# Kernel tuning notes

Hardware: AMD Instinct MI355X
Metric: run time of the kernel (lower is better)

Reference implementation:

```python
import jax, jax.numpy as jnp
import numpy as np

GRID_SIZE = 5
SPLINE_ORDER = 3
B, D, O = 16384, 512, 512


def _make_grid():
    h = 2.0 / GRID_SIZE
    # matches torch.arange(-k, grid_size + k + 1) * h - 2.0  -> 12 knots
    return jnp.arange(-SPLINE_ORDER, GRID_SIZE + SPLINE_ORDER + 1, dtype=jnp.float32) * h - 2.0


def _bspline_basis(x, grid):
    # x: [B, D]; grid: [G] with G = grid_size + 2*order + 1 = 12
    G = grid.shape[0]
    xe = x[..., None]                      # [B, D, 1]
    g = grid.reshape(1, 1, G)              # [1, 1, G]
    # degree-0: indicator of knot interval  -> [B, D, G-1]
    bases = ((xe >= g[:, :, :-1]) & (xe < g[:, :, 1:])).astype(x.dtype)
    eps = 1e-9
    for k in range(1, SPLINE_ORDER + 1):   # Cox-de Boor recursion, width shrinks by 1 each step
        left = (xe - g[:, :, :-k - 1]) / (g[:, :, k:-1] - g[:, :, :-k - 1] + eps)
        right = (g[:, :, k + 1:] - xe) / (g[:, :, k + 1:] - g[:, :, 1:-k] + eps)
        bases = left * bases[..., :-1] + right * bases[..., 1:]
    return bases                           # [B, D, grid_size + order] = [B, D, 8]


def setup_inputs() -> dict:
    key = jax.random.key(0)
    k1, k2, k3 = jax.random.split(key, 3)
    x = jax.random.normal(k1, (B, D), dtype=jnp.float32)
    # kaiming_uniform_(a=sqrt(5)*0.1): bound = sqrt(6 / ((1 + a^2) * fan_in))
    a = np.sqrt(5.0) * 0.1
    bound = float(np.sqrt(6.0 / ((1.0 + a * a) * D)))
    base_weight = jax.random.uniform(k2, (O, D), dtype=jnp.float32, minval=-bound, maxval=bound)
    spline_weight = jax.random.normal(k3, (O, D, GRID_SIZE + SPLINE_ORDER), dtype=jnp.float32) * 0.01
    return {"x": x, "base_weight": base_weight, "spline_weight": spline_weight}


def reference(x, base_weight, spline_weight):
    grid = _make_grid()
    base_output = jnp.matmul(jax.nn.silu(x), base_weight.T)      # [B, O]
    x_norm = jnp.clip(x, -2.0, 2.0)
    basis = _bspline_basis(x_norm, grid)                          # [B, D, 8]
    spline_output = jnp.einsum('bic,oic->bo', basis, spline_weight)
    return base_output + spline_output
```

## Files before the change

kernel.cpp:

```cpp
#include <hip/hip_runtime.h>
#include <cstdint>
#include <cstddef>
#include <type_traits>

#define B_ROWS 16384
#define D_DIM  512
#define O_DIM  512
#define K_DIM  4608
#define BM 64
#define BN 256
#define BK 32

typedef __bf16 bf16;
typedef __attribute__((ext_vector_type(8))) bf16  bf16x8;
typedef __attribute__((ext_vector_type(4))) float f32x4;

__device__ __forceinline__ void async_load16(const void* g, void* l) {
    __builtin_amdgcn_global_load_lds(
        (const __attribute__((address_space(1))) void*)g,
        (__attribute__((address_space(3))) void*)l,
        16, 0, 0);
}

__device__ __forceinline__ uint32_t pk2(float a, float b) {
    uint16_t ua = __builtin_bit_cast(uint16_t, (__bf16)a);
    uint16_t ub = __builtin_bit_cast(uint16_t, (__bf16)b);
    return (uint32_t)ua | ((uint32_t)ub << 16);
}

__device__ __forceinline__ void spline_pairs(float xv, uint32_t out[4]) {
    float xn = fminf(fmaxf(xv, -2.0f), 2.0f);
    float t  = (xn + 3.2f) * 2.5f;
    int   j0 = (int)t;
    float u  = t - (float)j0;
    float u2 = u * u, u3 = u2 * u, omu = 1.0f - u;
    const float s6 = 1.0f / 6.0f;
    float w0 = omu * omu * omu * s6;
    float w1 = (3.0f * u3 - 6.0f * u2 + 4.0f) * s6;
    float w2 = (-3.0f * u3 + 3.0f * u2 + 3.0f * u + 1.0f) * s6;
    float w3 = u3 * s6;
    uint64_t W64 = ((uint64_t)pk2(w2, w3) << 32) | pk2(w0, w1);
    int sh = (j0 - 3) * 16;
    uint64_t lo = W64 << (sh & 63);
    uint64_t hi = W64 >> ((64 - sh) & 63);
    uint32_t lo_lo = (uint32_t)lo, lo_hi = (uint32_t)(lo >> 32);
    uint32_t hi_lo = (uint32_t)hi, hi_hi = (uint32_t)(hi >> 32);
    bool lt64 = sh < 64, eq0 = (sh == 0), lt128 = sh < 128;
    out[0] = lt64 ? lo_lo : 0u;
    out[1] = lt64 ? lo_hi : 0u;
    out[2] = lt64 ? (eq0 ? 0u : hi_lo) : (lt128 ? lo_lo : 0u);
    out[3] = lt64 ? (eq0 ? 0u : hi_hi) : (lt128 ? lo_hi : 0u);
}

__global__ void pack_w_kernel(const float* __restrict__ bw,
                              const float* __restrict__ sw,
                              bf16* __restrict__ W) {
    int idx = blockIdx.x * blockDim.x + threadIdx.x;
    if (idx >= O_DIM * 64) return;
    int o  = idx >> 6;
    int i0 = (idx & 63) * 8;

    bf16 ob[9][8];
    const float* bwp = bw + (size_t)o * D_DIM + i0;
#pragma unroll
    for (int e = 0; e < 8; e++) {
        ob[0][e] = (bf16)bwp[e];
        const float* sp = sw + ((size_t)o * D_DIM + i0 + e) * 8;
#pragma unroll
        for (int c = 0; c < 8; c++)
            ob[c + 1][e] = (bf16)sp[c];
    }
    bf16* row = W + (size_t)o * K_DIM + i0;
#pragma unroll
    for (int f = 0; f < 9; f++)
        *(bf16x8*)(row + (size_t)f * D_DIM) = *(const bf16x8*)ob[f];
}

__global__ __launch_bounds__(512, 4)
void gemm_fused_kernel(const float* __restrict__ x, const bf16* __restrict__ W,
                       float* __restrict__ C) {
    __shared__ __align__(16) bf16 As[2][BM * BK];
    __shared__ __align__(16) bf16 Bs[2][BN * BK];

    const int tid  = threadIdx.x;
    const int n0   = blockIdx.x * BN;
    const int m0   = blockIdx.y * BM;
    const int wave = tid >> 6;
    const int lane = tid & 63;
    const int wn   = wave * 32;
    const int l15  = lane & 15;
    const int quad = lane >> 4;

    const int rA = tid >> 3;
    const int q8 = tid & 7;
    const float* xrow = x + (size_t)(m0 + rA) * D_DIM + q8 * 4;
    const int ps = (q8 >> 1) ^ ((rA >> 1) & 3);
    const int hh = q8 & 1;
    bf16* aw0 = &As[0][rA * BK + ps * 8 + hh * 4];
    bf16* aw1 = &As[1][rA * BK + ps * 8 + hh * 4];

    const int sr = tid >> 2;
    const int sc = ((tid & 3) ^ ((sr >> 1) & 3)) * 8;
    const bf16* gB = W + (size_t)(n0 + sr) * K_DIM + sc;
    bf16* lb0 = &Bs[0][tid * 8];
    bf16* lb1 = &Bs[1][tid * 8];

    const int swz  = (l15 >> 1) & 3;
    const int aoff = l15 * BK + (quad ^ swz) * 8;
    const int boff = (wn + l15) * BK + (quad ^ swz) * 8;

    f32x4 acc[4][2] = {};
    uint32_t vpk[2][4][4];
    float xe[4];

    {
        float4 a = *(const float4*)xrow;
        xe[0]=a.x; xe[1]=a.y; xe[2]=a.z; xe[3]=a.w;
#pragma unroll
        for (int e = 0; e < 4; e++) {
            uint32_t o4[4];
            spline_pairs(xe[e], o4);
            vpk[0][0][e]=o4[0]; vpk[0][1][e]=o4[1];
            vpk[0][2][e]=o4[2]; vpk[0][3][e]=o4[3];
        }
        float sl[4];
#pragma unroll
        for (int e = 0; e < 4; e++)
            sl[e] = xe[e] * __builtin_amdgcn_rcpf(1.0f + __expf(-xe[e]));
        uint32_t o[2] = {pk2(sl[0],sl[1]), pk2(sl[2],sl[3])};
        *(uint2*)aw0 = *(const uint2*)o;
        async_load16(gB, lb0);
        async_load16(gB + (size_t)128 * K_DIM, lb0 + 4096);
    }
    __syncthreads();

    auto chunk_body = [&](auto pcv, int c) {
        constexpr int PC = decltype(pcv)::value;
#pragma unroll
        for (int f = 0; f < 9; f++) {
            const int cur = (PC + f) & 1;
            const bf16* Asr = As[cur];
            const bf16* Bsr = Bs[cur];
            bf16* lbn = cur ? lb0 : lb1;
            bf16* awn = cur ? aw0 : aw1;
            const bool haveNext = !(c == 15 && f == 8);

            if (haveNext) {
                int koff = (f < 8) ? ((f + 1) * D_DIM + c * 32) : ((c + 1) * 32);
                async_load16(gB + koff, lbn);
                async_load16(gB + (size_t)128 * K_DIM + koff, lbn + 4096);
            }
            if (f == 0 && c < 15) {
                float4 a = *(const float4*)(xrow + (c + 1) * 32);
                xe[0]=a.x; xe[1]=a.y; xe[2]=a.z; xe[3]=a.w;
            }
            if (f >= 1 && f <= 4 && c < 15) {
                uint32_t o4[4];
                spline_pairs(xe[f - 1], o4);
                vpk[PC ^ 1][0][f-1]=o4[0]; vpk[PC ^ 1][1][f-1]=o4[1];
                vpk[PC ^ 1][2][f-1]=o4[2]; vpk[PC ^ 1][3][f-1]=o4[3];
            }
            if (haveNext) {
                uint32_t o[2];
                if (f < 8) {
                    const int pr = f >> 1;
#pragma unroll
                    for (int m = 0; m < 2; m++) {
                        uint32_t lo = vpk[PC][pr][2*m], hi = vpk[PC][pr][2*m+1];
                        o[m] = (f & 1) ? ((lo >> 16) | (hi & 0xFFFF0000u))
                                       : ((lo & 0xFFFFu) | (hi << 16));
                    }
                } else {
                    float sl[4];
#pragma unroll
                    for (int e = 0; e < 4; e++)
                        sl[e] = xe[e] * __builtin_amdgcn_rcpf(1.0f + __expf(-xe[e]));
                    o[0] = pk2(sl[0],sl[1]); o[1] = pk2(sl[2],sl[3]);
                }
                *(uint2*)awn = *(const uint2*)o;
            }

            bf16x8 af[4], bfr[2];
#pragma unroll
            for (int tt = 0; tt < 4; tt++)
                af[tt] = *(const bf16x8*)(Asr + aoff + tt * 16 * BK);
#pragma unroll
            for (int jn = 0; jn < 2; jn++)
                bfr[jn] = *(const bf16x8*)(Bsr + boff + jn * 16 * BK);
#pragma unroll
            for (int im = 0; im < 4; im++)
#pragma unroll
                for (int jn = 0; jn < 2; jn++)
                    acc[im][jn] = __builtin_amdgcn_mfma_f32_16x16x32_bf16(
                        af[im], bfr[jn], acc[im][jn], 0, 0, 0);
            __syncthreads();
        }
    };

    for (int cc = 0; cc < 16; cc += 2) {
        chunk_body(std::integral_constant<int,0>{}, cc);
        chunk_body(std::integral_constant<int,1>{}, cc + 1);
    }

#pragma unroll
    for (int im = 0; im < 4; im++) {
        const int rbase = m0 + im * 16 + quad * 4;
#pragma unroll
        for (int jn = 0; jn < 2; jn++) {
            const int col = n0 + wn + jn * 16 + l15;
#pragma unroll
            for (int rr = 0; rr < 4; rr++)
                C[(size_t)(rbase + rr) * O_DIM + col] = acc[im][jn][rr];
        }
    }
}

extern "C" void kernel_launch(void* const* d_in, const int* in_sizes, int n_in,
                              void* d_out, int out_size, void* d_ws, size_t ws_size,
                              hipStream_t stream) {
    const float* x  = (const float*)d_in[0];
    const float* bw = (const float*)d_in[1];
    const float* sw = (const float*)d_in[2];
    float* out = (float*)d_out;

    const size_t Wbytes = (size_t)O_DIM * K_DIM * sizeof(bf16);
    if (ws_size < Wbytes) return;
    bf16* W = (bf16*)d_ws;

    pack_w_kernel<<<(O_DIM * 64 + 255) / 256, 256, 0, stream>>>(bw, sw, W);
    gemm_fused_kernel<<<dim3(O_DIM / BN, B_ROWS / BM), 512, 0, stream>>>(x, W, out);
}
```

Baseline: 187.6 us.

## Load weight fragments directly into registers and cover all columns per block

The fused GEMM now gives each block a 32-row tile that spans all 512 output columns. Each wave reads its weight MFMA fragments straight from global memory into double-buffered registers, and the B tile no longer goes through LDS. This removes the LDS staging traffic for weights and computes each spline basis value only once per row instead of once per column tile. In exchange, every block re-reads the whole weight matrix through the cache with less reuse per load, and the global-load latency is now exposed in the register pipeline.

Result: slower. 349.2 us (+86.1%).

```diff
diff --git a/kernel.cpp b/kernel.cpp
--- a/kernel.cpp
+++ b/kernel.cpp
@@ -7,20 +7,11 @@
 #define D_DIM  512
 #define O_DIM  512
 #define K_DIM  4608
-#define BM 64
-#define BN 256
-#define BK 32
+#define BM 32
 
 typedef __bf16 bf16;
 typedef __attribute__((ext_vector_type(8))) bf16  bf16x8;
 typedef __attribute__((ext_vector_type(4))) float f32x4;
-
-__device__ __forceinline__ void async_load16(const void* g, void* l) {
-    __builtin_amdgcn_global_load_lds(
-        (const __attribute__((address_space(1))) void*)g,
-        (__attribute__((address_space(3))) void*)l,
-        16, 0, 0);
-}
 
 __device__ __forceinline__ uint32_t pk2(float a, float b) {
     uint16_t ua = __builtin_bit_cast(uint16_t, (__bf16)a);
@@ -79,58 +70,45 @@
 __global__ __launch_bounds__(512, 4)
 void gemm_fused_kernel(const float* __restrict__ x, const bf16* __restrict__ W,
                        float* __restrict__ C) {
-    __shared__ __align__(16) bf16 As[2][BM * BK];
-    __shared__ __align__(16) bf16 Bs[2][BN * BK];
+    __shared__ __align__(16) bf16 As[2][BM * 32];
 
     const int tid  = threadIdx.x;
-    const int n0   = blockIdx.x * BN;
-    const int m0   = blockIdx.y * BM;
+    const int m0   = blockIdx.x * BM;
     const int wave = tid >> 6;
     const int lane = tid & 63;
-    const int wn   = wave * 32;
+    const int wn   = wave * 64;
     const int l15  = lane & 15;
     const int quad = lane >> 4;
 
-    const int rA = tid >> 3;
-    const int q8 = tid & 7;
-    const float* xrow = x + (size_t)(m0 + rA) * D_DIM + q8 * 4;
-    const int ps = (q8 >> 1) ^ ((rA >> 1) & 3);
-    const int hh = q8 & 1;
-    bf16* aw0 = &As[0][rA * BK + ps * 8 + hh * 4];
-    bf16* aw1 = &As[1][rA * BK + ps * 8 + hh * 4];
+    const int r  = tid >> 4;
+    const int ip = tid & 15;
+    const float* xp = x + (size_t)(m0 + r) * D_DIM + ip * 2;
+    const int awo = r * 32 + (((ip >> 2) ^ ((r >> 1) & 3)) << 3) + (ip & 3) * 2;
 
-    const int sr = tid >> 2;
-    const int sc = ((tid & 3) ^ ((sr >> 1) & 3)) * 8;
-    const bf16* gB = W + (size_t)(n0 + sr) * K_DIM + sc;
-    bf16* lb0 = &Bs[0][tid * 8];
-    bf16* lb1 = &Bs[1][tid * 8];
+    const bf16* wp0 = W + (size_t)(wn +  0 + l15) * K_DIM + quad * 8;
+    const bf16* wp1 = W + (size_t)(wn + 16 + l15) * K_DIM + quad * 8;
+    const bf16* wp2 = W + (size_t)(wn + 32 + l15) * K_DIM + quad * 8;
+    const bf16* wp3 = W + (size_t)(wn + 48 + l15) * K_DIM + quad * 8;
 
-    const int swz  = (l15 >> 1) & 3;
-    const int aoff = l15 * BK + (quad ^ swz) * 8;
-    const int boff = (wn + l15) * BK + (quad ^ swz) * 8;
+    const int aoff = l15 * 32 + ((quad ^ ((l15 >> 1) & 3)) << 3);
 
-    f32x4 acc[4][2] = {};
-    uint32_t vpk[2][4][4];
-    float xe[4];
+    f32x4 acc[2][4] = {};
+    bf16x8 wfr[2][4];
+    uint32_t vpk[2][2][4];
+    float xe[2];
 
     {
-        float4 a = *(const float4*)xrow;
-        xe[0]=a.x; xe[1]=a.y; xe[2]=a.z; xe[3]=a.w;
-#pragma unroll
-        for (int e = 0; e < 4; e++) {
-            uint32_t o4[4];
-            spline_pairs(xe[e], o4);
-            vpk[0][0][e]=o4[0]; vpk[0][1][e]=o4[1];
-            vpk[0][2][e]=o4[2]; vpk[0][3][e]=o4[3];
-        }
-        float sl[4];
-#pragma unroll
-        for (int e = 0; e < 4; e++)
-            sl[e] = xe[e] * __builtin_amdgcn_rcpf(1.0f + __expf(-xe[e]));
-        uint32_t o[2] = {pk2(sl[0],sl[1]), pk2(sl[2],sl[3])};
-        *(uint2*)aw0 = *(const uint2*)o;
-        async_load16(gB, lb0);
-        async_load16(gB + (size_t)128 * K_DIM, lb0 + 4096);
+        float2 xv = *(const float2*)xp;
+        xe[0] = xv.x; xe[1] = xv.y;
+        spline_pairs(xe[0], vpk[0][0]);
+        spline_pairs(xe[1], vpk[0][1]);
+        float s0 = xe[0] * __builtin_amdgcn_rcpf(1.0f + __expf(-xe[0]));
+        float s1 = xe[1] * __builtin_amdgcn_rcpf(1.0f + __expf(-xe[1]));
+        *(uint32_t*)&As[0][awo] = pk2(s0, s1);
+        wfr[0][0] = *(const bf16x8*)wp0;
+        wfr[0][1] = *(const bf16x8*)wp1;
+        wfr[0][2] = *(const bf16x8*)wp2;
+        wfr[0][3] = *(const bf16x8*)wp3;
     }
     __syncthreads();
 
@@ -139,60 +117,46 @@
 #pragma unroll
         for (int f = 0; f < 9; f++) {
             const int cur = (PC + f) & 1;
-            const bf16* Asr = As[cur];
-            const bf16* Bsr = Bs[cur];
-            bf16* lbn = cur ? lb0 : lb1;
-            bf16* awn = cur ? aw0 : aw1;
+            const int nxt = cur ^ 1;
             const bool haveNext = !(c == 15 && f == 8);
 
             if (haveNext) {
-                int koff = (f < 8) ? ((f + 1) * D_DIM + c * 32) : ((c + 1) * 32);
-                async_load16(gB + koff, lbn);
-                async_load16(gB + (size_t)128 * K_DIM + koff, lbn + 4096);
+                const int koff = (f < 8) ? ((f + 1) * D_DIM + c * 32)
+                                         : ((c + 1) * 32);
+                wfr[nxt][0] = *(const bf16x8*)(wp0 + koff);
+                wfr[nxt][1] = *(const bf16x8*)(wp1 + koff);
+                wfr[nxt][2] = *(const bf16x8*)(wp2 + koff);
+                wfr[nxt][3] = *(const bf16x8*)(wp3 + koff);
             }
             if (f == 0 && c < 15) {
-                float4 a = *(const float4*)(xrow + (c + 1) * 32);
-                xe[0]=a.x; xe[1]=a.y; xe[2]=a.z; xe[3]=a.w;
+                float2 xv = *(const float2*)(xp + (c + 1) * 32);
+                xe[0] = xv.x; xe[1] = xv.y;
             }
-            if (f >= 1 && f <= 4 && c < 15) {
-                uint32_t o4[4];
-                spline_pairs(xe[f - 1], o4);
-                vpk[PC ^ 1][0][f-1]=o4[0]; vpk[PC ^ 1][1][f-1]=o4[1];
-                vpk[PC ^ 1][2][f-1]=o4[2]; vpk[PC ^ 1][3][f-1]=o4[3];
-            }
+            if ((f == 1 || f == 2) && c < 15)
+                spline_pairs(xe[f - 1], vpk[PC ^ 1][f - 1]);
             if (haveNext) {
-                uint32_t o[2];
+                uint32_t o;
                 if (f < 8) {
-                    const int pr = f >> 1;
-#pragma unroll
-                    for (int m = 0; m < 2; m++) {
-                        uint32_t lo = vpk[PC][pr][2*m], hi = vpk[PC][pr][2*m+1];
-                        o[m] = (f & 1) ? ((lo >> 16) | (hi & 0xFFFF0000u))
-                                       : ((lo & 0xFFFFu) | (hi << 16));
-                    }
+                    uint32_t lo = vpk[PC][0][f >> 1], hi = vpk[PC][1][f >> 1];
+                    o = (f & 1) ? ((lo >> 16) | (hi & 0xFFFF0000u))
+                                : ((lo & 0xFFFFu) | (hi << 16));
                 } else {
-                    float sl[4];
-#pragma unroll
-                    for (int e = 0; e < 4; e++)
-                        sl[e] = xe[e] * __builtin_amdgcn_rcpf(1.0f + __expf(-xe[e]));
-                    o[0] = pk2(sl[0],sl[1]); o[1] = pk2(sl[2],sl[3]);
+                    float s0 = xe[0] * __builtin_amdgcn_rcpf(1.0f + __expf(-xe[0]));
+                    float s1 = xe[1] * __builtin_amdgcn_rcpf(1.0f + __expf(-xe[1]));
+                    o = pk2(s0, s1);
                 }
-                *(uint2*)awn = *(const uint2*)o;
+                *(uint32_t*)&As[nxt][awo] = o;
             }
 
-            bf16x8 af[4], bfr[2];
+            bf16x8 af[2];
+            af[0] = *(const bf16x8*)(&As[cur][aoff]);
+            af[1] = *(const bf16x8*)(&As[cur][aoff + 512]);
 #pragma unroll
-            for (int tt = 0; tt < 4; tt++)
-                af[tt] = *(const bf16x8*)(Asr + aoff + tt * 16 * BK);
+            for (int tt = 0; tt < 2; tt++)
 #pragma unroll
-            for (int jn = 0; jn < 2; jn++)
-                bfr[jn] = *(const bf16x8*)(Bsr + boff + jn * 16 * BK);
-#pragma unroll
-            for (int im = 0; im < 4; im++)
-#pragma unroll
-                for (int jn = 0; jn < 2; jn++)
-                    acc[im][jn] = __builtin_amdgcn_mfma_f32_16x16x32_bf16(
-                        af[im], bfr[jn], acc[im][jn], 0, 0, 0);
+                for (int jn = 0; jn < 4; jn++)
+                    acc[tt][jn] = __builtin_amdgcn_mfma_f32_16x16x32_bf16(
+                        af[tt], wfr[cur][jn], acc[tt][jn], 0, 0, 0);
             __syncthreads();
         }
     };
@@ -203,14 +167,14 @@
     }
 
 #pragma unroll
-    for (int im = 0; im < 4; im++) {
-        const int rbase = m0 + im * 16 + quad * 4;
+    for (int tt = 0; tt < 2; tt++) {
+        const int rbase = m0 + tt * 16 + quad * 4;
 #pragma unroll
-        for (int jn = 0; jn < 2; jn++) {
-            const int col = n0 + wn + jn * 16 + l15;
+        for (int jn = 0; jn < 4; jn++) {
+            const int col = wn + jn * 16 + l15;
 #pragma unroll
             for (int rr = 0; rr < 4; rr++)
-                C[(size_t)(rbase + rr) * O_DIM + col] = acc[im][jn][rr];
+                C[(size_t)(rbase + rr) * O_DIM + col] = acc[tt][jn][rr];
         }
     }
 }
@@ -228,5 +192,5 @@
     bf16* W = (bf16*)d_ws;
 
     pack_w_kernel<<<(O_DIM * 64 + 255) / 256, 256, 0, stream>>>(bw, sw, W);
-    gemm_fused_kernel<<<dim3(O_DIM / BN, B_ROWS / BM), 512, 0, stream>>>(x, W, out);
+    gemm_fused_kernel<<<dim3(B_ROWS / BM), 512, 0, stream>>>(x, W, out);
 }
```
